# Kernel optimization log

Hardware: AMD Instinct MI355X
Metric: run time of the kernel (lower is better)

Reference implementation:

```python
import jax, jax.numpy as jnp
import numpy as np

B, L, D = 4, 2048, 1024
DI = D            # d_inner = expand * d_model, expand=1
N = 8             # d_state
K = 4             # d_conv
R = 64            # dt_rank = ceil(d_model/16)
EPS = 1e-5


def setup_inputs() -> dict:
    key = jax.random.key(0)
    ks = jax.random.split(key, 10)
    hidden_states = jax.random.normal(ks[0], (B, L, D), dtype=jnp.float32)
    norm_w = jnp.ones((D,), dtype=jnp.float32)
    in_proj_w = jax.random.normal(ks[1], (2 * DI, D), dtype=jnp.float32) * 0.02
    conv_w = jax.random.normal(ks[2], (DI, 1, K), dtype=jnp.float32) * 0.2
    conv_b = jnp.zeros((DI,), dtype=jnp.float32)
    x_proj_w = jax.random.normal(ks[3], (R + 2 * N, DI), dtype=jnp.float32) * 0.02
    dt_proj_w = jax.random.normal(ks[4], (DI, R), dtype=jnp.float32) * 0.1
    # bias init so softplus(bias) lands in a sane dt range (~e^-4 .. e^-1)
    dt_proj_b = jax.random.uniform(ks[5], (DI,), minval=-4.0, maxval=-1.0, dtype=jnp.float32)
    # S4D-real style init: A = -[1..N] per channel
    A_log = jnp.log(jnp.broadcast_to(jnp.arange(1, N + 1, dtype=jnp.float32), (DI, N)))
    D_skip = jnp.ones((DI,), dtype=jnp.float32)
    out_proj_w = jax.random.normal(ks[6], (D, DI), dtype=jnp.float32) * 0.02
    return {
        "hidden_states": hidden_states, "norm_w": norm_w,
        "in_proj_w": in_proj_w, "conv_w": conv_w, "conv_b": conv_b,
        "x_proj_w": x_proj_w, "dt_proj_w": dt_proj_w, "dt_proj_b": dt_proj_b,
        "A_log": A_log, "D_skip": D_skip, "out_proj_w": out_proj_w,
    }


def _rmsnorm(x, w):
    return x * jax.lax.rsqrt(jnp.mean(x * x, axis=-1, keepdims=True) + EPS) * w


def _mamba_block(hidden_states, norm_w, in_proj_w, conv_w, conv_b,
                 x_proj_w, dt_proj_w, dt_proj_b, A_log, D_skip, out_proj_w):
    x = _rmsnorm(hidden_states, norm_w)                      # [B,L,D]
    xz = jnp.einsum('bld,ed->ble', x, in_proj_w)             # [B,L,2*DI]
    x, z = jnp.split(xz, 2, axis=-1)                         # [B,L,DI] each
    # causal depthwise conv1d (torch pads d_conv-1 both sides then slices :L => left pad only)
    xc = jnp.transpose(x, (0, 2, 1))                         # [B,DI,L]
    k = conv_w.shape[-1]
    xc = jax.lax.conv_general_dilated(
        xc, conv_w, window_strides=(1,), padding=[(k - 1, 0)],
        dimension_numbers=('NCH', 'OIH', 'NCH'), feature_group_count=DI)
    x = jax.nn.silu(jnp.transpose(xc, (0, 2, 1)) + conv_b)   # [B,L,DI]
    # input-dependent dt, B, C
    dbl = jnp.einsum('bld,ed->ble', x, x_proj_w)             # [B,L,R+2N]
    dt, Bm, Cm = jnp.split(dbl, [R, R + N], axis=-1)
    dt = jax.nn.softplus(jnp.einsum('blr,dr->bld', dt, dt_proj_w) + dt_proj_b)  # [B,L,DI]
    A = -jnp.exp(A_log)                                      # [DI,N]
    dA = jnp.exp(dt[..., None] * A)                          # [B,L,DI,N]
    dBx = dt[..., None] * Bm[:, :, None, :] * x[..., None]   # [B,L,DI,N]

    def step(h, inp):
        a_t, bx_t, c_t = inp                                 # [B,DI,N],[B,DI,N],[B,N]
        h = a_t * h + bx_t
        y = jnp.einsum('bdn,bn->bd', h, c_t)
        return h, y

    h0 = jnp.zeros((hidden_states.shape[0], DI, N), dtype=x.dtype)
    _, ys = jax.lax.scan(step, h0, (jnp.transpose(dA, (1, 0, 2, 3)),
                                    jnp.transpose(dBx, (1, 0, 2, 3)),
                                    jnp.transpose(Cm, (1, 0, 2))))
    y = jnp.transpose(ys, (1, 0, 2)) + D_skip * x            # [B,L,DI]
    y = y * jax.nn.silu(z)
    out = jnp.einsum('bld,ed->ble', y, out_proj_w)           # [B,L,D]
    return out  # use_res=False


def reference(hidden_states, norm_w, in_proj_w, conv_w, conv_b,
              x_proj_w, dt_proj_w, dt_proj_b, A_log, D_skip, out_proj_w):
    return _mamba_block(hidden_states, norm_w, in_proj_w, conv_w, conv_b,
                        x_proj_w, dt_proj_w, dt_proj_b, A_log, D_skip, out_proj_w)
```

## Files before the change

### kernel.cpp

```cpp
#include <hip/hip_runtime.h>
#include <stdint.h>
#include <stddef.h>


typedef unsigned short u16;
typedef unsigned int u32;
typedef _Float16 f16;
typedef __attribute__((ext_vector_type(8))) _Float16 half8;
typedef __attribute__((ext_vector_type(4))) _Float16 half4;
typedef __attribute__((ext_vector_type(4))) float f32x4;

#define LSEQ 2048
#define DMODEL 1024
#define NSTATE 8
#define NCHUNK 64
#define CHUNKL 32
#define NROWS 8192
#define WS_NEED (115ull << 20)

__device__ __forceinline__ void gload_lds16(const void* g, void* l) {
    __builtin_amdgcn_global_load_lds((__attribute__((address_space(1))) void*)g,
                                     (__attribute__((address_space(3))) void*)l,
                                     16, 0, 0);
}

__global__ __launch_bounds__(256) void sentinel_kernel(float* __restrict__ out, int n) {
    int i = blockIdx.x * 256 + threadIdx.x;
    if (i < n) out[i] = 999.0f;
}

#define T0 524288
#define T1 20480
#define T2 16384
#define T3 262144
#define WCVT_BLK 3216
#define ZERO_BLK 640
__global__ __launch_bounds__(256) void prep_kernel(const float* __restrict__ s0,
                                                   const float* __restrict__ s1,
                                                   const float* __restrict__ s2,
                                                   const float* __restrict__ s3,
                                                   f16* __restrict__ d0, f16* __restrict__ d1,
                                                   f16* __restrict__ d2, f16* __restrict__ d3,
                                                   float* __restrict__ dblz,
                                                   const float* __restrict__ X,
                                                   const float* __restrict__ W,
                                                   f16* __restrict__ O) {
    const int bx = blockIdx.x;
    const int tid = threadIdx.x;
    if (bx < WCVT_BLK) {
        int idx = bx * 256 + tid;
        const float* s; f16* d; int i;
        if (idx < T0) { s = s0; d = d0; i = idx; }
        else if (idx < T0 + T1) { s = s1; d = d1; i = idx - T0; }
        else if (idx < T0 + T1 + T2) { s = s2; d = d2; i = idx - T0 - T1; }
        else { s = s3; d = d3; i = idx - T0 - T1 - T2; }
        f32x4 v = *(const f32x4*)(s + (size_t)i * 4);
        half4 o; o[0] = (f16)v[0]; o[1] = (f16)v[1]; o[2] = (f16)v[2]; o[3] = (f16)v[3];
        *(half4*)(d + (size_t)i * 4) = o;
    } else if (bx < WCVT_BLK + ZERO_BLK) {
        int i = (bx - WCVT_BLK) * 256 + tid;
        const f32x4 z4 = {0.f, 0.f, 0.f, 0.f};
        ((f32x4*)dblz)[i] = z4;
    } else {
        const int row = bx - (WCVT_BLK + ZERO_BLK);
        f32x4 u = *(const f32x4*)(X + (size_t)row * DMODEL + tid * 4);
        float ss = u[0]*u[0] + u[1]*u[1] + u[2]*u[2] + u[3]*u[3];
        for (int off = 32; off; off >>= 1) ss += __shfl_down(ss, off, 64);
        __shared__ float red[4];
        if ((tid & 63) == 0) red[tid >> 6] = ss;
        __syncthreads();
        float tot = red[0] + red[1] + red[2] + red[3];
        float scale = rsqrtf(tot * (1.0f / DMODEL) + 1e-5f);
        f32x4 w = *(const f32x4*)(W + tid * 4);
        half4 o;
        o[0] = (f16)(u[0] * scale * w[0]); o[1] = (f16)(u[1] * scale * w[1]);
        o[2] = (f16)(u[2] * scale * w[2]); o[3] = (f16)(u[3] * scale * w[3]);
        *(half4*)(O + (size_t)row * DMODEL + tid * 4) = o;
    }
}

template <int EPI, int AF32>
__global__ __launch_bounds__(256) void gemm_f16(const void* __restrict__ Ap, int lda,
                                                const f16* __restrict__ Bm, int ldb,
                                                void* __restrict__ C0, void* __restrict__ C1,
                                                int ldc, int N, int klen,
                                                const float* __restrict__ fbias) {
    __shared__ alignas(16) f16 sA[128 * 64];
    __shared__ alignas(16) f16 sB[128 * 64];
    const int tid = threadIdx.x;
    const int wave = tid >> 6, lane = tid & 63;
    const int wm = (wave >> 1) * 64, wn = (wave & 1) * 64;
    const int tm = blockIdx.x, tn = blockIdx.y;
    const int q = lane >> 4, cl = lane & 15;
    const int kbeg = blockIdx.z * klen;

    f32x4 acc[4][4];
    const f32x4 zero4 = {0.f, 0.f, 0.f, 0.f};
#pragma unroll
    for (int t = 0; t < 4; t++)
#pragma unroll
        for (int u = 0; u < 4; u++) acc[t][u] = zero4;

    int rS[4], gkS[4];
#pragma unroll
    for (int j = 0; j < 4; j++) {
        int c = wave * 256 + j * 64 + lane;
        rS[j] = c >> 3;
        gkS[j] = (c & 7) ^ (rS[j] & 7);
    }

    for (int k0 = kbeg; k0 < kbeg + klen; k0 += 64) {
        __syncthreads();
#pragma unroll
        for (int j = 0; j < 4; j++) {
            int ldsoff = (wave * 256 + j * 64) * 8;
            if (!AF32) {
                int ga = tm * 128 + rS[j];
                gload_lds16((const f16*)Ap + (size_t)ga * lda + k0 + gkS[j] * 8, sA + ldsoff);
            }
            int gb = tn * 128 + rS[j];
            if (gb >= N) gb = N - 1;
            gload_lds16(Bm + (size_t)gb * ldb + k0 + gkS[j] * 8, sB + ldsoff);
        }
        __syncthreads();

        half8 af[4][2], bf[4][2];
#pragma unroll
        for (int t = 0; t < 4; t++)
#pragma unroll
            for (int s = 0; s < 2; s++) {
                int m = wm + t * 16 + cl;
                int kc = s * 4 + q;
                if (AF32) {
                    const float* pa = (const float*)Ap + (size_t)(tm * 128 + m) * lda + k0 + kc * 8;
                    f32x4 v0 = *(const f32x4*)pa, v1 = *(const f32x4*)(pa + 4);
                    half8 a;
                    a[0] = (f16)v0[0]; a[1] = (f16)v0[1]; a[2] = (f16)v0[2]; a[3] = (f16)v0[3];
                    a[4] = (f16)v1[0]; a[5] = (f16)v1[1]; a[6] = (f16)v1[2]; a[7] = (f16)v1[3];
                    af[t][s] = a;
                } else {
                    af[t][s] = *(const half8*)(sA + m * 64 + ((kc ^ (m & 7)) << 3));
                }
                int n = wn + t * 16 + cl;
                bf[t][s] = *(const half8*)(sB + n * 64 + ((kc ^ (n & 7)) << 3));
            }
#pragma unroll
        for (int t = 0; t < 4; t++)
#pragma unroll
            for (int u = 0; u < 4; u++) {
                acc[t][u] = __builtin_amdgcn_mfma_f32_16x16x32_f16(af[t][0], bf[u][0], acc[t][u], 0, 0, 0);
                acc[t][u] = __builtin_amdgcn_mfma_f32_16x16x32_f16(af[t][1], bf[u][1], acc[t][u], 0, 0, 0);
            }
    }

    const int rowbase = tm * 128 + wm + q * 4;
    const int colbase = tn * 128 + wn + cl;
#pragma unroll
    for (int t = 0; t < 4; t++)
#pragma unroll
        for (int r = 0; r < 4; r++) {
            size_t rb_ = (size_t)(rowbase + t * 16 + r) * ldc;
            size_t rb1 = (size_t)(rowbase + t * 16 + r) * 1024;
#pragma unroll
            for (int u = 0; u < 4; u++) {
                int gcol = colbase + u * 16;
                float v = acc[t][u][r];
                if (EPI == 0) {
                    if (gcol < 1024) ((f16*)C0)[rb1 + gcol] = (f16)v;
                    else             ((f16*)C1)[rb1 + gcol - 1024] = (f16)v;
                } else if (EPI == 1) {
                    if (gcol < N) ((float*)C0)[rb_ + gcol] = v;
                } else if (EPI == 2) {
                    if (gcol < N) atomicAdd((float*)C0 + rb_ + gcol, v);
                } else {
                    if (gcol < N) {
                        float sv = v + fbias[gcol];
                        sv = (sv > 15.f) ? sv : log1pf(__expf(sv));
                        ((f16*)C0)[rb_ + gcol] = (f16)sv;
                    }
                }
            }
        }
}

__global__ __launch_bounds__(256) void conv_silu_kernel(const f16* __restrict__ x,
                                                        const float* __restrict__ cw,
                                                        const float* __restrict__ cb,
                                                        f16* __restrict__ xc) {
    const int rg = blockIdx.x;
    const int d = blockIdx.y * 256 + threadIdx.x;
    const int row0 = rg * 4;
    const int l0 = row0 & (LSEQ - 1);
    float w0 = cw[d * 4], w1 = cw[d * 4 + 1], w2 = cw[d * 4 + 2], w3 = cw[d * 4 + 3];
    float bias = cb[d];
    float v[7];
#pragma unroll
    for (int j = 0; j < 7; j++) {
        int ll = l0 - 3 + j;
        v[j] = (ll >= 0) ? (float)x[(size_t)(row0 - 3 + j) * 1024 + d] : 0.f;
    }
#pragma unroll
    for (int i = 0; i < 4; i++) {
        float acc = bias + w0 * v[i] + w1 * v[i + 1] + w2 * v[i + 2] + w3 * v[i + 3];
        xc[(size_t)(row0 + i) * 1024 + d] = (f16)(acc / (1.f + __expf(-acc)));
    }
}

__global__ __launch_bounds__(256) void scan1_kernel(const f16* __restrict__ dt,
                                                    const f16* __restrict__ xc,
                                                    const float* __restrict__ dbl,
                                                    const float* __restrict__ A_log,
                                                    float* __restrict__ hF,
                                                    float* __restrict__ Pb) {
    const int d = blockIdx.x * 256 + threadIdx.x;
    const int c = blockIdx.y;
    const int b = blockIdx.z;
    __shared__ float sB[CHUNKL * NSTATE];
    sB[threadIdx.x] = dbl[(size_t)(b * LSEQ + c * CHUNKL + (threadIdx.x >> 3)) * 80 + 64 + (threadIdx.x & 7)];
    __syncthreads();
    f32x4 al0 = *(const f32x4*)(A_log + d * 8);
    f32x4 al1 = *(const f32x4*)(A_log + d * 8 + 4);
    float Aa[NSTATE];
#pragma unroll
    for (int n = 0; n < 4; n++) { Aa[n] = -__expf(al0[n]); Aa[n + 4] = -__expf(al1[n]); }
    float h[NSTATE], P[NSTATE];
#pragma unroll
    for (int n = 0; n < NSTATE; n++) { h[n] = 0.f; P[n] = 1.f; }
    const f16* pdt = dt + (size_t)(b * LSEQ + c * CHUNKL) * 1024 + d;
    const f16* pxc = xc + (size_t)(b * LSEQ + c * CHUNKL) * 1024 + d;
    for (int lb = 0; lb < CHUNKL; lb += 8) {
        float vdt[8], vxc[8];
#pragma unroll
        for (int j = 0; j < 8; j++) {
            vdt[j] = (float)pdt[(size_t)(lb + j) * 1024];
            vxc[j] = (float)pxc[(size_t)(lb + j) * 1024];
        }
#pragma unroll
        for (int j = 0; j < 8; j++) {
            float dtx = vdt[j] * vxc[j];
#pragma unroll
            for (int n = 0; n < NSTATE; n++) {
                float e = __expf(Aa[n] * vdt[j]);
                h[n] = e * h[n] + dtx * sB[(lb + j) * 8 + n];
                P[n] *= e;
            }
        }
    }
    size_t base = ((size_t)(c * 4 + b) * 1024 + d) * 8;
    f32x4 o;
    o[0]=h[0]; o[1]=h[1]; o[2]=h[2]; o[3]=h[3]; *(f32x4*)(hF + base) = o;
    o[0]=h[4]; o[1]=h[5]; o[2]=h[6]; o[3]=h[7]; *(f32x4*)(hF + base + 4) = o;
    o[0]=P[0]; o[1]=P[1]; o[2]=P[2]; o[3]=P[3]; *(f32x4*)(Pb + base) = o;
    o[0]=P[4]; o[1]=P[5]; o[2]=P[6]; o[3]=P[7]; *(f32x4*)(Pb + base + 4) = o;
}

__global__ __launch_bounds__(256) void combine_kernel(const float* __restrict__ hF,
                                                      const float* __restrict__ Pb,
                                                      float* __restrict__ h0) {
    int t = blockIdx.x * 256 + threadIdx.x;
    int n = t & 7, dd = (t >> 3) & 1023, b = t >> 13;
    size_t off = (size_t)(b * 1024 + dd) * 8 + n;
    float h = 0.f;
#pragma unroll 8
    for (int c = 0; c < NCHUNK; c++) {
        size_t idx = (size_t)c * 32768 + off;
        h0[idx] = h;
        h = fmaf(Pb[idx], h, hF[idx]);
    }
}

__global__ __launch_bounds__(256) void scan2_kernel(const f16* __restrict__ dt,
                                                    const f16* __restrict__ xc,
                                                    const float* __restrict__ dbl,
                                                    const float* __restrict__ A_log,
                                                    const float* __restrict__ h0,
                                                    const f16* __restrict__ z,
                                                    const float* __restrict__ Dsk,
                                                    f16* __restrict__ yout) {
    const int d = blockIdx.x * 256 + threadIdx.x;
    const int c = blockIdx.y;
    const int b = blockIdx.z;
    __shared__ float sB[CHUNKL * NSTATE];
    __shared__ float sC[CHUNKL * NSTATE];
    {
        size_t rb = (size_t)(b * LSEQ + c * CHUNKL + (threadIdx.x >> 3)) * 80;
        sB[threadIdx.x] = dbl[rb + 64 + (threadIdx.x & 7)];
        sC[threadIdx.x] = dbl[rb + 72 + (threadIdx.x & 7)];
    }
    __syncthreads();
    f32x4 al0 = *(const f32x4*)(A_log + d * 8);
    f32x4 al1 = *(const f32x4*)(A_log + d * 8 + 4);
    float Aa[NSTATE];
#pragma unroll
    for (int n = 0; n < 4; n++) { Aa[n] = -__expf(al0[n]); Aa[n + 4] = -__expf(al1[n]); }
    float h[NSTATE];
    {
        size_t base = ((size_t)(c * 4 + b) * 1024 + d) * 8;
        f32x4 h0a = *(const f32x4*)(h0 + base);
        f32x4 h0b = *(const f32x4*)(h0 + base + 4);
#pragma unroll
        for (int n = 0; n < 4; n++) { h[n] = h0a[n]; h[n + 4] = h0b[n]; }
    }
    const float dval = Dsk[d];
    const size_t rowoff = (size_t)(b * LSEQ + c * CHUNKL) * 1024 + d;
    const f16* pdt = dt + rowoff;
    const f16* pxc = xc + rowoff;
    const f16* pz  = z  + rowoff;
    f16* py = yout + rowoff;
    for (int lb = 0; lb < CHUNKL; lb += 8) {
        float vdt[8], vxc[8], vz[8];
#pragma unroll
        for (int j = 0; j < 8; j++) {
            vdt[j] = (float)pdt[(size_t)(lb + j) * 1024];
            vxc[j] = (float)pxc[(size_t)(lb + j) * 1024];
            vz[j]  = (float)pz[(size_t)(lb + j) * 1024];
        }
#pragma unroll
        for (int j = 0; j < 8; j++) {
            float dtx = vdt[j] * vxc[j];
            float y = 0.f;
#pragma unroll
            for (int n = 0; n < NSTATE; n++) {
                float e = __expf(Aa[n] * vdt[j]);
                h[n] = e * h[n] + dtx * sB[(lb + j) * 8 + n];
                y += h[n] * sC[(lb + j) * 8 + n];
            }
            y += dval * vxc[j];
            y *= vz[j] / (1.f + __expf(-vz[j]));
            py[(size_t)(lb + j) * 1024] = (f16)y;
        }
    }
}

extern "C" void kernel_launch(void* const* d_in, const int* in_sizes, int n_in,
                              void* d_out, int out_size, void* d_ws, size_t ws_size,
                              hipStream_t stream) {
    (void)in_sizes; (void)n_in;
    const float* hidden    = (const float*)d_in[0];
    const float* norm_w    = (const float*)d_in[1];
    const float* in_proj_w = (const float*)d_in[2];
    const float* conv_w    = (const float*)d_in[3];
    const float* conv_b    = (const float*)d_in[4];
    const float* x_proj_w  = (const float*)d_in[5];
    const float* dt_proj_w = (const float*)d_in[6];
    const float* dt_proj_b = (const float*)d_in[7];
    const float* A_log     = (const float*)d_in[8];
    const float* D_skip    = (const float*)d_in[9];
    const float* out_proj_w= (const float*)d_in[10];
    float* out = (float*)d_out;

    if (ws_size < WS_NEED) {
        sentinel_kernel<<<dim3((out_size + 255) / 256), 256, 0, stream>>>(out, out_size);
        return;
    }

    char* ws = (char*)d_ws;
    f16*   xn_h  = (f16*)(ws);
    f16*   xbuf_h= (f16*)(ws + (16ull << 20));
    f16*   zbuf_h= (f16*)(ws + (32ull << 20));
    f16*   xc_h  = (f16*)(ws + (48ull << 20));
    f16*   wih   = (f16*)(ws + (64ull << 20));
    f16*   woh   = (f16*)(ws + (68ull << 20));
    f16*   wxh   = (f16*)(ws + (70ull << 20));
    f16*   wdh   = (f16*)(ws + (70ull << 20) + (512ull << 10));
    float* dbl_f = (float*)(ws + (71ull << 20));
    f16*   dth   = (f16*)(ws + (75ull << 20));
    float* hF    = (float*)(ws + (91ull << 20));
    float* Pb    = (float*)(ws + (99ull << 20));
    float* h0    = (float*)(ws + (107ull << 20));
    f16*   y_h   = xn_h;

    prep_kernel<<<dim3(WCVT_BLK + ZERO_BLK + NROWS), 256, 0, stream>>>(
        in_proj_w, x_proj_w, dt_proj_w, out_proj_w, wih, wxh, wdh, woh,
        dbl_f, hidden, norm_w, xn_h);
    gemm_f16<0, 0><<<dim3(64, 16), 256, 0, stream>>>(xn_h, 1024, wih, 1024,
                                                     xbuf_h, zbuf_h, 1024, 2048, 1024, nullptr);
    conv_silu_kernel<<<dim3(NROWS / 4, 4), 256, 0, stream>>>(xbuf_h, conv_w, conv_b, xc_h);
    gemm_f16<2, 0><<<dim3(64, 1, 4), 256, 0, stream>>>(xc_h, 1024, wxh, 1024,
                                                       dbl_f, nullptr, 80, 80, 256, nullptr);
    gemm_f16<3, 1><<<dim3(64, 8), 256, 0, stream>>>(dbl_f, 80, wdh, 64,
                                                    dth, nullptr, 1024, 1024, 64, dt_proj_b);
    scan1_kernel<<<dim3(4, NCHUNK, 4), 256, 0, stream>>>(dth, xc_h, dbl_f, A_log, hF, Pb);
    combine_kernel<<<dim3(128), 256, 0, stream>>>(hF, Pb, h0);
    scan2_kernel<<<dim3(4, NCHUNK, 4), 256, 0, stream>>>(dth, xc_h, dbl_f, A_log, h0,
                                                         zbuf_h, D_skip, y_h);
    gemm_f16<1, 0><<<dim3(64, 8), 256, 0, stream>>>(y_h, 1024, woh, 1024,
                                                    out, nullptr, 1024, 1024, 1024, nullptr);
}
```

Before: 295.8 us.

## Fuse causal conv+SiLU into x_proj GEMM and scans, fold chunk combine into scan2

Removes the standalone conv_silu kernel and the xc buffer. The conv+SiLU is now recomputed on the fly from the raw x buffer inside the x_proj GEMM A-operand load and inside both scan kernels. It also drops the combine kernel: each scan2 block serially folds the per-chunk (P, hF) carries of all preceding chunks to get its initial state. This saves two launches and an 8192x1024 f16 write and reread, in exchange for redundant conv/exp work, uncoalesced A loads from global in the GEMM, and O(chunks) carry reads per scan2 block.

```diff
diff --git a/kernel.cpp b/kernel.cpp
--- a/kernel.cpp
+++ b/kernel.cpp
@@ -16,7 +16,7 @@
 #define NCHUNK 64
 #define CHUNKL 32
 #define NROWS 8192
-#define WS_NEED (115ull << 20)
+#define WS_NEED (107ull << 20)
 
 __device__ __forceinline__ void gload_lds16(const void* g, void* l) {
     __builtin_amdgcn_global_load_lds((__attribute__((address_space(1))) void*)g,
@@ -79,12 +79,14 @@
     }
 }
 
-template <int EPI, int AF32>
+template <int EPI, int AMODE>
 __global__ __launch_bounds__(256) void gemm_f16(const void* __restrict__ Ap, int lda,
                                                 const f16* __restrict__ Bm, int ldb,
                                                 void* __restrict__ C0, void* __restrict__ C1,
                                                 int ldc, int N, int klen,
-                                                const float* __restrict__ fbias) {
+                                                const float* __restrict__ fbias,
+                                                const float* __restrict__ cw,
+                                                const float* __restrict__ cb) {
     __shared__ alignas(16) f16 sA[128 * 64];
     __shared__ alignas(16) f16 sB[128 * 64];
     const int tid = threadIdx.x;
@@ -114,7 +116,7 @@
 #pragma unroll
         for (int j = 0; j < 4; j++) {
             int ldsoff = (wave * 256 + j * 64) * 8;
-            if (!AF32) {
+            if (AMODE == 0) {
                 int ga = tm * 128 + rS[j];
                 gload_lds16((const f16*)Ap + (size_t)ga * lda + k0 + gkS[j] * 8, sA + ldsoff);
             }
@@ -125,20 +127,57 @@
         __syncthreads();
 
         half8 af[4][2], bf[4][2];
+        if (AMODE == 2) {
+#pragma unroll
+            for (int s = 0; s < 2; s++) {
+                int kch = k0 + (s * 4 + q) * 8;
+                float cwv[4][8], cbv[8];
+#pragma unroll
+                for (int e = 0; e < 8; e++) {
+                    f32x4 c4 = *(const f32x4*)(cw + (size_t)(kch + e) * 4);
+                    cwv[0][e] = c4[0]; cwv[1][e] = c4[1]; cwv[2][e] = c4[2]; cwv[3][e] = c4[3];
+                    cbv[e] = cb[kch + e];
+                }
+#pragma unroll
+                for (int t = 0; t < 4; t++) {
+                    int m = tm * 128 + wm + t * 16 + cl;
+                    int l = m & (LSEQ - 1);
+                    half8 xr[4];
+#pragma unroll
+                    for (int jj = 0; jj < 4; jj++) {
+                        if (l - 3 + jj >= 0)
+                            xr[jj] = *(const half8*)((const f16*)Ap + (size_t)(m - 3 + jj) * lda + kch);
+                        else {
+                            half8 zz = {0, 0, 0, 0, 0, 0, 0, 0};
+                            xr[jj] = zz;
+                        }
+                    }
+                    half8 a;
+#pragma unroll
+                    for (int e = 0; e < 8; e++) {
+                        float v = cbv[e] + cwv[0][e] * (float)xr[0][e] + cwv[1][e] * (float)xr[1][e]
+                                + cwv[2][e] * (float)xr[2][e] + cwv[3][e] * (float)xr[3][e];
+                        v = v / (1.f + __expf(-v));
+                        a[e] = (f16)v;
+                    }
+                    af[t][s] = a;
+                }
+            }
+        }
 #pragma unroll
         for (int t = 0; t < 4; t++)
 #pragma unroll
             for (int s = 0; s < 2; s++) {
                 int m = wm + t * 16 + cl;
                 int kc = s * 4 + q;
-                if (AF32) {
+                if (AMODE == 1) {
                     const float* pa = (const float*)Ap + (size_t)(tm * 128 + m) * lda + k0 + kc * 8;
                     f32x4 v0 = *(const f32x4*)pa, v1 = *(const f32x4*)(pa + 4);
                     half8 a;
                     a[0] = (f16)v0[0]; a[1] = (f16)v0[1]; a[2] = (f16)v0[2]; a[3] = (f16)v0[3];
                     a[4] = (f16)v1[0]; a[5] = (f16)v1[1]; a[6] = (f16)v1[2]; a[7] = (f16)v1[3];
                     af[t][s] = a;
-                } else {
+                } else if (AMODE == 0) {
                     af[t][s] = *(const half8*)(sA + m * 64 + ((kc ^ (m & 7)) << 3));
                 }
                 int n = wn + t * 16 + cl;
@@ -183,33 +222,12 @@
         }
 }
 
-__global__ __launch_bounds__(256) void conv_silu_kernel(const f16* __restrict__ x,
-                                                        const float* __restrict__ cw,
-                                                        const float* __restrict__ cb,
-                                                        f16* __restrict__ xc) {
-    const int rg = blockIdx.x;
-    const int d = blockIdx.y * 256 + threadIdx.x;
-    const int row0 = rg * 4;
-    const int l0 = row0 & (LSEQ - 1);
-    float w0 = cw[d * 4], w1 = cw[d * 4 + 1], w2 = cw[d * 4 + 2], w3 = cw[d * 4 + 3];
-    float bias = cb[d];
-    float v[7];
-#pragma unroll
-    for (int j = 0; j < 7; j++) {
-        int ll = l0 - 3 + j;
-        v[j] = (ll >= 0) ? (float)x[(size_t)(row0 - 3 + j) * 1024 + d] : 0.f;
-    }
-#pragma unroll
-    for (int i = 0; i < 4; i++) {
-        float acc = bias + w0 * v[i] + w1 * v[i + 1] + w2 * v[i + 2] + w3 * v[i + 3];
-        xc[(size_t)(row0 + i) * 1024 + d] = (f16)(acc / (1.f + __expf(-acc)));
-    }
-}
-
 __global__ __launch_bounds__(256) void scan1_kernel(const f16* __restrict__ dt,
-                                                    const f16* __restrict__ xc,
+                                                    const f16* __restrict__ xb,
                                                     const float* __restrict__ dbl,
                                                     const float* __restrict__ A_log,
+                                                    const float* __restrict__ cw,
+                                                    const float* __restrict__ cb,
                                                     float* __restrict__ hF,
                                                     float* __restrict__ Pb) {
     const int d = blockIdx.x * 256 + threadIdx.x;
@@ -223,21 +241,31 @@
     float Aa[NSTATE];
 #pragma unroll
     for (int n = 0; n < 4; n++) { Aa[n] = -__expf(al0[n]); Aa[n + 4] = -__expf(al1[n]); }
+    f32x4 cwv = *(const f32x4*)(cw + d * 4);
+    const float cbv = cb[d];
     float h[NSTATE], P[NSTATE];
 #pragma unroll
     for (int n = 0; n < NSTATE; n++) { h[n] = 0.f; P[n] = 1.f; }
-    const f16* pdt = dt + (size_t)(b * LSEQ + c * CHUNKL) * 1024 + d;
-    const f16* pxc = xc + (size_t)(b * LSEQ + c * CHUNKL) * 1024 + d;
+    const size_t rowoff = (size_t)(b * LSEQ + c * CHUNKL) * 1024 + d;
+    const f16* pdt = dt + rowoff;
+    const f16* px = xb + rowoff;
+    float xm3 = 0.f, xm2 = 0.f, xm1 = 0.f;
+    if (c > 0) {
+        xm3 = (float)px[-3 * 1024]; xm2 = (float)px[-2 * 1024]; xm1 = (float)px[-1 * 1024];
+    }
     for (int lb = 0; lb < CHUNKL; lb += 8) {
-        float vdt[8], vxc[8];
+        float vdt[8], vx[8];
 #pragma unroll
         for (int j = 0; j < 8; j++) {
             vdt[j] = (float)pdt[(size_t)(lb + j) * 1024];
-            vxc[j] = (float)pxc[(size_t)(lb + j) * 1024];
+            vx[j] = (float)px[(size_t)(lb + j) * 1024];
         }
 #pragma unroll
         for (int j = 0; j < 8; j++) {
-            float dtx = vdt[j] * vxc[j];
+            float cv = cbv + cwv[0] * xm3 + cwv[1] * xm2 + cwv[2] * xm1 + cwv[3] * vx[j];
+            xm3 = xm2; xm2 = xm1; xm1 = vx[j];
+            float xv = cv / (1.f + __expf(-cv));
+            float dtx = vdt[j] * xv;
 #pragma unroll
             for (int n = 0; n < NSTATE; n++) {
                 float e = __expf(Aa[n] * vdt[j]);
@@ -254,26 +282,14 @@
     o[0]=P[4]; o[1]=P[5]; o[2]=P[6]; o[3]=P[7]; *(f32x4*)(Pb + base + 4) = o;
 }
 
-__global__ __launch_bounds__(256) void combine_kernel(const float* __restrict__ hF,
-                                                      const float* __restrict__ Pb,
-                                                      float* __restrict__ h0) {
-    int t = blockIdx.x * 256 + threadIdx.x;
-    int n = t & 7, dd = (t >> 3) & 1023, b = t >> 13;
-    size_t off = (size_t)(b * 1024 + dd) * 8 + n;
-    float h = 0.f;
-#pragma unroll 8
-    for (int c = 0; c < NCHUNK; c++) {
-        size_t idx = (size_t)c * 32768 + off;
-        h0[idx] = h;
-        h = fmaf(Pb[idx], h, hF[idx]);
-    }
-}
-
 __global__ __launch_bounds__(256) void scan2_kernel(const f16* __restrict__ dt,
-                                                    const f16* __restrict__ xc,
+                                                    const f16* __restrict__ xb,
                                                     const float* __restrict__ dbl,
                                                     const float* __restrict__ A_log,
-                                                    const float* __restrict__ h0,
+                                                    const float* __restrict__ hF,
+                                                    const float* __restrict__ Pb,
+                                                    const float* __restrict__ cw,
+                                                    const float* __restrict__ cb,
                                                     const f16* __restrict__ z,
                                                     const float* __restrict__ Dsk,
                                                     f16* __restrict__ yout) {
@@ -294,30 +310,48 @@
 #pragma unroll
     for (int n = 0; n < 4; n++) { Aa[n] = -__expf(al0[n]); Aa[n + 4] = -__expf(al1[n]); }
     float h[NSTATE];
+#pragma unroll
+    for (int n = 0; n < NSTATE; n++) h[n] = 0.f;
     {
-        size_t base = ((size_t)(c * 4 + b) * 1024 + d) * 8;
-        f32x4 h0a = *(const f32x4*)(h0 + base);
-        f32x4 h0b = *(const f32x4*)(h0 + base + 4);
-#pragma unroll
-        for (int n = 0; n < 4; n++) { h[n] = h0a[n]; h[n + 4] = h0b[n]; }
-    }
+        size_t off = ((size_t)b * 1024 + d) * 8;
+#pragma unroll 4
+        for (int cc = 0; cc < c; cc++) {
+            size_t base = (size_t)cc * 32768 + off;
+            f32x4 p0 = *(const f32x4*)(Pb + base), p1 = *(const f32x4*)(Pb + base + 4);
+            f32x4 g0 = *(const f32x4*)(hF + base), g1 = *(const f32x4*)(hF + base + 4);
+#pragma unroll
+            for (int n = 0; n < 4; n++) {
+                h[n] = fmaf(p0[n], h[n], g0[n]);
+                h[n + 4] = fmaf(p1[n], h[n + 4], g1[n]);
+            }
+        }
+    }
+    f32x4 cwv = *(const f32x4*)(cw + d * 4);
+    const float cbv = cb[d];
     const float dval = Dsk[d];
     const size_t rowoff = (size_t)(b * LSEQ + c * CHUNKL) * 1024 + d;
     const f16* pdt = dt + rowoff;
-    const f16* pxc = xc + rowoff;
-    const f16* pz  = z  + rowoff;
+    const f16* px = xb + rowoff;
+    const f16* pz = z + rowoff;
     f16* py = yout + rowoff;
+    float xm3 = 0.f, xm2 = 0.f, xm1 = 0.f;
+    if (c > 0) {
+        xm3 = (float)px[-3 * 1024]; xm2 = (float)px[-2 * 1024]; xm1 = (float)px[-1 * 1024];
+    }
     for (int lb = 0; lb < CHUNKL; lb += 8) {
-        float vdt[8], vxc[8], vz[8];
+        float vdt[8], vx[8], vz[8];
 #pragma unroll
         for (int j = 0; j < 8; j++) {
             vdt[j] = (float)pdt[(size_t)(lb + j) * 1024];
-            vxc[j] = (float)pxc[(size_t)(lb + j) * 1024];
-            vz[j]  = (float)pz[(size_t)(lb + j) * 1024];
+            vx[j] = (float)px[(size_t)(lb + j) * 1024];
+            vz[j] = (float)pz[(size_t)(lb + j) * 1024];
         }
 #pragma unroll
         for (int j = 0; j < 8; j++) {
-            float dtx = vdt[j] * vxc[j];
+            float cv = cbv + cwv[0] * xm3 + cwv[1] * xm2 + cwv[2] * xm1 + cwv[3] * vx[j];
+            xm3 = xm2; xm2 = xm1; xm1 = vx[j];
+            float xv = cv / (1.f + __expf(-cv));
+            float dtx = vdt[j] * xv;
             float y = 0.f;
 #pragma unroll
             for (int n = 0; n < NSTATE; n++) {
@@ -325,7 +359,7 @@
                 h[n] = e * h[n] + dtx * sB[(lb + j) * 8 + n];
                 y += h[n] * sC[(lb + j) * 8 + n];
             }
-            y += dval * vxc[j];
+            y += dval * xv;
             y *= vz[j] / (1.f + __expf(-vz[j]));
             py[(size_t)(lb + j) * 1024] = (f16)y;
         }
@@ -358,7 +392,6 @@
     f16*   xn_h  = (f16*)(ws);
     f16*   xbuf_h= (f16*)(ws + (16ull << 20));
     f16*   zbuf_h= (f16*)(ws + (32ull << 20));
-    f16*   xc_h  = (f16*)(ws + (48ull << 20));
     f16*   wih   = (f16*)(ws + (64ull << 20));
     f16*   woh   = (f16*)(ws + (68ull << 20));
     f16*   wxh   = (f16*)(ws + (70ull << 20));
@@ -367,23 +400,25 @@
     f16*   dth   = (f16*)(ws + (75ull << 20));
     float* hF    = (float*)(ws + (91ull << 20));
     float* Pb    = (float*)(ws + (99ull << 20));
-    float* h0    = (float*)(ws + (107ull << 20));
     f16*   y_h   = xn_h;
 
     prep_kernel<<<dim3(WCVT_BLK + ZERO_BLK + NROWS), 256, 0, stream>>>(
         in_proj_w, x_proj_w, dt_proj_w, out_proj_w, wih, wxh, wdh, woh,
         dbl_f, hidden, norm_w, xn_h);
     gemm_f16<0, 0><<<dim3(64, 16), 256, 0, stream>>>(xn_h, 1024, wih, 1024,
-                                                     xbuf_h, zbuf_h, 1024, 2048, 1024, nullptr);
-    conv_silu_kernel<<<dim3(NROWS / 4, 4), 256, 0, stream>>>(xbuf_h, conv_w, conv_b, xc_h);
-    gemm_f16<2, 0><<<dim3(64, 1, 4), 256, 0, stream>>>(xc_h, 1024, wxh, 1024,
-                                                       dbl_f, nullptr, 80, 80, 256, nullptr);
+                                                     xbuf_h, zbuf_h, 1024, 2048, 1024,
+                                                     nullptr, nullptr, nullptr);
+    gemm_f16<2, 2><<<dim3(64, 1, 4), 256, 0, stream>>>(xbuf_h, 1024, wxh, 1024,
+                                                       dbl_f, nullptr, 80, 80, 256,
+                                                       nullptr, conv_w, conv_b);
     gemm_f16<3, 1><<<dim3(64, 8), 256, 0, stream>>>(dbl_f, 80, wdh, 64,
-                                                    dth, nullptr, 1024, 1024, 64, dt_proj_b);
-    scan1_kernel<<<dim3(4, NCHUNK, 4), 256, 0, stream>>>(dth, xc_h, dbl_f, A_log, hF, Pb);
-    combine_kernel<<<dim3(128), 256, 0, stream>>>(hF, Pb, h0);
-    scan2_kernel<<<dim3(4, NCHUNK, 4), 256, 0, stream>>>(dth, xc_h, dbl_f, A_log, h0,
-                                                         zbuf_h, D_skip, y_h);
+                                                    dth, nullptr, 1024, 1024, 64,
+                                                    dt_proj_b, nullptr, nullptr);
+    scan1_kernel<<<dim3(4, NCHUNK, 4), 256, 0, stream>>>(dth, xbuf_h, dbl_f, A_log,
+                                                         conv_w, conv_b, hF, Pb);
+    scan2_kernel<<<dim3(4, NCHUNK, 4), 256, 0, stream>>>(dth, xbuf_h, dbl_f, A_log, hF, Pb,
+                                                         conv_w, conv_b, zbuf_h, D_skip, y_h);
     gemm_f16<1, 0><<<dim3(64, 8), 256, 0, stream>>>(y_h, 1024, woh, 1024,
-                                                    out, nullptr, 1024, 1024, 1024, nullptr);
-}
+                                                    out, nullptr, 1024, 1024, 1024,
+                                                    nullptr, nullptr, nullptr);
+}
```

Result: slower. 330.8 us (+11.8%).
